# Performance work log

Measured on AMD Instinct MI355X. Metric: run time of the kernel, lower is better.

Reference implementation:

```python
import jax, jax.numpy as jnp
import numpy as np

EPS = 1e-8  # torch.nn.CosineSimilarity default eps


def setup_inputs() -> dict:
    key = jax.random.key(0)
    ks = jax.random.split(key, 6)
    B, N, SD, HD, AD = 512, 256, 1024, 512, 256
    return {
        "state_emb": jax.random.normal(ks[0], (B, SD), dtype=jnp.float32),
        "hints_emb": jax.random.normal(ks[1], (B, N, HD), dtype=jnp.float32),
        "Ws": jax.random.normal(ks[2], (AD, SD), dtype=jnp.float32) * 0.02,
        "bs": jax.random.normal(ks[3], (AD,), dtype=jnp.float32) * 0.02,
        "Wh": jax.random.normal(ks[4], (AD, HD), dtype=jnp.float32) * 0.02,
        "bh": jax.random.normal(ks[5], (AD,), dtype=jnp.float32) * 0.02,
    }


def reference(state_emb, hints_emb, Ws, bs, Wh, bh):
    # Projections
    sp = state_emb @ Ws.T + bs                       # (B, A)
    hp = jnp.einsum("bnh,ah->bna", hints_emb, Wh) + bh  # (B, N, A)
    # Cosine similarity along feature dim (torch CosineSimilarity semantics)
    sn = jnp.maximum(jnp.linalg.norm(sp, axis=-1, keepdims=True), EPS)    # (B,1)
    hn = jnp.maximum(jnp.linalg.norm(hp, axis=-1), EPS)                   # (B,N)
    scores = jnp.einsum("ba,bna->bn", sp, hp) / (sn * hn)                 # (B,N)
    attn_weights = jax.nn.softmax(scores, axis=1)                         # (B,N)
    # Weighted sum over hints (original, unprojected embeddings)
    output = jnp.einsum("bn,bnh->bh", attn_weights, hints_emb)            # (B,HD)
    return output
```

## Files before the change

### kernel.cpp

```cpp
#include <hip/hip_runtime.h>
#include <hip/hip_bf16.h>

typedef __attribute__((ext_vector_type(8))) short bf16x8;
typedef __attribute__((ext_vector_type(4))) float f32x4;

#define B_  512
#define N_  256
#define SD_ 1024
#define HD_ 512
#define AD_ 256

__device__ __forceinline__ unsigned short f2bf(float f) {
    unsigned int u = __float_as_uint(f);
    unsigned int r = (u + 0x7FFFu + ((u >> 16) & 1u)) >> 16;
    return (unsigned short)r;
}

__global__ void k0_pack(const float* __restrict__ Wh, unsigned short* __restrict__ whp) {
    int g = blockIdx.x * 256 + threadIdx.x;
    int ct  = g >> 10;
    int rem = g & 1023;
    int ks  = rem >> 6;
    int l   = rem & 63;
    int a   = ct * 16 + (l & 15);
    int kb  = ks * 32 + (l >> 4) * 8;
    const float* src = Wh + (size_t)a * HD_ + kb;
    float4 v0 = *(const float4*)(src);
    float4 v1 = *(const float4*)(src + 4);
    bf16x8 o;
    o[0] = (short)f2bf(v0.x); o[1] = (short)f2bf(v0.y);
    o[2] = (short)f2bf(v0.z); o[3] = (short)f2bf(v0.w);
    o[4] = (short)f2bf(v1.x); o[5] = (short)f2bf(v1.y);
    o[6] = (short)f2bf(v1.z); o[7] = (short)f2bf(v1.w);
    ((bf16x8*)whp)[g] = o;
}

__global__ __launch_bounds__(512) void k1_proj(
    const float* __restrict__ state, const float* __restrict__ Ws,
    const float* __restrict__ bs,
    float* __restrict__ sn, float* __restrict__ spv)
{
    __shared__ float st[2][SD_];
    __shared__ float spl[2][AD_];
    __shared__ float red[2][AD_];
    int tid = threadIdx.x, lane = tid & 63, w = tid >> 6;
    int b0 = blockIdx.x * 2;
    ((float4*)st)[tid] = ((const float4*)(state + (size_t)b0 * SD_))[tid];
    __syncthreads();
    float4 s0[4], s1[4];
    #pragma unroll
    for (int seg = 0; seg < 4; ++seg) {
        s0[seg] = *(const float4*)&st[0][seg * 256 + lane * 4];
        s1[seg] = *(const float4*)&st[1][seg * 256 + lane * 4];
    }
    #pragma unroll 2
    for (int i = 0; i < 32; ++i) {
        int a = w * 32 + i;
        const float4* wr = (const float4*)(Ws + (size_t)a * SD_);
        float p0 = 0.f, p1 = 0.f;
        #pragma unroll
        for (int seg = 0; seg < 4; ++seg) {
            float4 wv = wr[seg * 64 + lane];
            p0 += wv.x * s0[seg].x + wv.y * s0[seg].y + wv.z * s0[seg].z + wv.w * s0[seg].w;
            p1 += wv.x * s1[seg].x + wv.y * s1[seg].y + wv.z * s1[seg].z + wv.w * s1[seg].w;
        }
        #pragma unroll
        for (int d = 1; d < 64; d <<= 1) { p0 += __shfl_xor(p0, d); p1 += __shfl_xor(p1, d); }
        if (lane == 0) {
            float bsa = bs[a];
            spl[0][a] = p0 + bsa;
            spl[1][a] = p1 + bsa;
        }
    }
    __syncthreads();
    int tb = tid >> 8, t = tid & 255;
    float sv = spl[tb][t];
    spv[(size_t)(b0 + tb) * AD_ + t] = sv;
    red[tb][t] = sv * sv;
    __syncthreads();
    for (int s = 128; s > 0; s >>= 1) { if (t < s) red[tb][t] += red[tb][t + s]; __syncthreads(); }
    if (t == 0) sn[b0 + tb] = fmaxf(sqrtf(red[tb][0]), 1e-8f);
}

__global__ __launch_bounds__(512, 2) void k2_fused(
    const float* __restrict__ hints, const unsigned short* __restrict__ whp,
    const float* __restrict__ spv, const float* __restrict__ sn,
    const float* __restrict__ bh, float* __restrict__ out)
{
    __shared__ __align__(16) char smem[74752];
    unsigned short* tile = (unsigned short*)smem;
    float* sp_lds  = (float*)(smem + 65536);
    float* bh_lds  = (float*)(smem + 66560);
    float* norm2p  = (float*)(smem + 67584);
    float* nump    = (float*)(smem + 69632);
    float* sc      = (float*)(smem + 71680);
    float* red     = (float*)(smem + 72704);
    float* wsm     = (float*)(smem + 73728);
    float* scratch = (float*)smem;

    int tid = threadIdx.x, lane = tid & 63, w = tid >> 6;
    int b = blockIdx.x;
    const float* hb = hints + (size_t)b * N_ * HD_;
    if (tid < 64) ((float4*)sp_lds)[tid] = ((const float4*)(spv + (size_t)b * AD_))[tid];
    else if (tid < 128) ((float4*)bh_lds)[tid - 64] = ((const float4*)bh)[tid - 64];
    float snb = sn[b];
    int cl = lane & 15;
    int srow = tid >> 3;
    int sseg = tid & 7;
    const float* srcrow = hb + (size_t)srow * HD_ + sseg * 64;
    __syncthreads();
    float bh0 = bh_lds[(2 * w + 0) * 16 + cl];
    float bh1 = bh_lds[(2 * w + 1) * 16 + cl];
    float sp0 = sp_lds[(2 * w + 0) * 16 + cl];
    float sp1 = sp_lds[(2 * w + 1) * 16 + cl];

    #pragma unroll 1
    for (int mc = 0; mc < 4; ++mc) {
        const float* src = srcrow + (size_t)(mc * 64) * HD_;
        #pragma unroll
        for (int h = 0; h < 2; ++h) {
            float4 v[8];
            #pragma unroll
            for (int j = 0; j < 8; ++j)
                v[j] = *(const float4*)(src + h * 32 + j * 4);
            #pragma unroll
            for (int j2 = 0; j2 < 4; ++j2) {
                int s = sseg * 8 + h * 4 + j2;
                int sw = s ^ (srow & 15);
                float4 a = v[2 * j2], c = v[2 * j2 + 1];
                bf16x8 pk;
                pk[0] = (short)f2bf(a.x); pk[1] = (short)f2bf(a.y);
                pk[2] = (short)f2bf(a.z); pk[3] = (short)f2bf(a.w);
                pk[4] = (short)f2bf(c.x); pk[5] = (short)f2bf(c.y);
                pk[6] = (short)f2bf(c.z); pk[7] = (short)f2bf(c.w);
                *(bf16x8*)((char*)tile + srow * 1024 + sw * 16) = pk;
            }
        }
        __syncthreads();

        f32x4 acc[4][2];
        #pragma unroll
        for (int mf = 0; mf < 4; ++mf) {
            acc[mf][0] = (f32x4){0.f, 0.f, 0.f, 0.f};
            acc[mf][1] = (f32x4){0.f, 0.f, 0.f, 0.f};
        }
        #pragma unroll
        for (int kidx = 0; kidx < 16; ++kidx) {
            bf16x8 bfr0 = ((const bf16x8*)whp)[((2 * w + 0) * 16 + kidx) * 64 + lane];
            bf16x8 bfr1 = ((const bf16x8*)whp)[((2 * w + 1) * 16 + kidx) * 64 + lane];
            #pragma unroll
            for (int mf = 0; mf < 4; ++mf) {
                int r = mf * 16 + cl;
                int s = kidx * 4 + (lane >> 4);
                bf16x8 afr = *(const bf16x8*)((const char*)tile + r * 1024 +
                                              ((s ^ (r & 15)) << 4));
                acc[mf][0] = __builtin_amdgcn_mfma_f32_16x16x32_bf16(afr, bfr0, acc[mf][0], 0, 0, 0);
                acc[mf][1] = __builtin_amdgcn_mfma_f32_16x16x32_bf16(afr, bfr1, acc[mf][1], 0, 0, 0);
            }
        }

        #pragma unroll
        for (int mf = 0; mf < 4; ++mf) {
            #pragma unroll
            for (int r = 0; r < 4; ++r) {
                float h0 = acc[mf][0][r] + bh0;
                float h1 = acc[mf][1][r] + bh1;
                float vv = h0 * h0 + h1 * h1;
                float uu = sp0 * h0 + sp1 * h1;
                vv += __shfl_xor(vv, 1); uu += __shfl_xor(uu, 1);
                vv += __shfl_xor(vv, 2); uu += __shfl_xor(uu, 2);
                vv += __shfl_xor(vv, 4); uu += __shfl_xor(uu, 4);
                vv += __shfl_xor(vv, 8); uu += __shfl_xor(uu, 8);
                if (cl == 0) {
                    int idx = w * 64 + mf * 16 + (lane >> 4) * 4 + r;
                    norm2p[idx] = vv;
                    nump[idx]   = uu;
                }
            }
        }
        __syncthreads();
        if (tid < 64) {
            float n2 = 0.f, nm = 0.f;
            #pragma unroll
            for (int ww = 0; ww < 8; ++ww) {
                n2 += norm2p[ww * 64 + tid];
                nm += nump[ww * 64 + tid];
            }
            float hn = fmaxf(sqrtf(n2), 1e-8f);
            sc[mc * 64 + tid] = nm / (snb * hn);
        }
    }
    __syncthreads();

    if (tid < 256) red[tid] = sc[tid];
    __syncthreads();
    for (int s = 128; s > 0; s >>= 1) { if (tid < s) red[tid] = fmaxf(red[tid], red[tid + s]); __syncthreads(); }
    float mx = red[0];
    __syncthreads();
    if (tid < 256) { float e = __expf(sc[tid] - mx); sc[tid] = e; red[tid] = e; }
    __syncthreads();
    for (int s = 128; s > 0; s >>= 1) { if (tid < s) red[tid] += red[tid + s]; __syncthreads(); }
    float inv = 1.f / red[0];
    __syncthreads();
    if (tid < 256) wsm[tid] = sc[tid] * inv;
    __syncthreads();

    int hg = tid & 127, ng = tid >> 7;
    const float* hbe = hb + (size_t)(ng * 64) * HD_ + hg * 4;
    float ax = 0.f, ay = 0.f, az = 0.f, aw = 0.f;
    #pragma unroll 8
    for (int n = 0; n < 64; ++n) {
        float4 hv = *(const float4*)(hbe + (size_t)n * HD_);
        float wn = wsm[ng * 64 + n];
        ax += wn * hv.x; ay += wn * hv.y; az += wn * hv.z; aw += wn * hv.w;
    }
    *(float4*)(scratch + ng * 512 + hg * 4) = (float4){ax, ay, az, aw};
    __syncthreads();
    out[(size_t)b * HD_ + tid] =
        scratch[tid] + scratch[512 + tid] + scratch[1024 + tid] + scratch[1536 + tid];
}

extern "C" void kernel_launch(void* const* d_in, const int* in_sizes, int n_in,
                              void* d_out, int out_size, void* d_ws, size_t ws_size,
                              hipStream_t stream) {
    const float* state = (const float*)d_in[0];
    const float* hints = (const float*)d_in[1];
    const float* Ws    = (const float*)d_in[2];
    const float* bs    = (const float*)d_in[3];
    const float* Wh    = (const float*)d_in[4];
    const float* bh    = (const float*)d_in[5];
    float* out = (float*)d_out;

    float* sn = (float*)d_ws;
    float* spv = sn + B_;
    unsigned short* whp = (unsigned short*)(spv + (size_t)B_ * AD_);

    k0_pack<<<64, 256, 0, stream>>>(Wh, whp);
    k1_proj<<<B_ / 2, 512, 0, stream>>>(state, Ws, bs, sn, spv);
    k2_fused<<<B_, 512, 0, stream>>>(hints, whp, spv, sn, bh, out);
}
```

Baseline: 165.6 us.

## Split fused kernel into score and weighted-sum kernels with direct-register A loads

Replaces the single per-batch fused kernel with two kernels. The first runs four blocks per batch, each loading 64 hint rows straight from global memory into MFMA A fragments, converting them with the packed bf16 instruction instead of staging through LDS. The second does the softmax and weighted sum per batch. This adds parallelism and removes the LDS tile and its barriers. In exchange the hints tensor is read twice from HBM in separate launches, and the scores take an extra round trip through the workspace.

```diff
diff --git a/kernel.cpp b/kernel.cpp
--- a/kernel.cpp
+++ b/kernel.cpp
@@ -3,6 +3,7 @@
 
 typedef __attribute__((ext_vector_type(8))) short bf16x8;
 typedef __attribute__((ext_vector_type(4))) float f32x4;
+typedef __attribute__((ext_vector_type(4))) unsigned int u32x4;
 
 #define B_  512
 #define N_  256
@@ -14,6 +15,12 @@
     unsigned int u = __float_as_uint(f);
     unsigned int r = (u + 0x7FFFu + ((u >> 16) & 1u)) >> 16;
     return (unsigned short)r;
+}
+
+__device__ __forceinline__ unsigned int cvtpk(float lo, float hi) {
+    unsigned int r;
+    asm("v_cvt_pk_bf16_f32 %0, %1, %2" : "=v"(r) : "v"(lo), "v"(hi));
+    return r;
 }
 
 __global__ void k0_pack(const float* __restrict__ Wh, unsigned short* __restrict__ whp) {
@@ -82,116 +89,104 @@
     if (t == 0) sn[b0 + tb] = fmaxf(sqrtf(red[tb][0]), 1e-8f);
 }
 
-__global__ __launch_bounds__(512, 2) void k2_fused(
+__global__ __launch_bounds__(256, 3) void k2_scores(
     const float* __restrict__ hints, const unsigned short* __restrict__ whp,
     const float* __restrict__ spv, const float* __restrict__ sn,
-    const float* __restrict__ bh, float* __restrict__ out)
+    const float* __restrict__ bh, float* __restrict__ scores)
 {
-    __shared__ __align__(16) char smem[74752];
-    unsigned short* tile = (unsigned short*)smem;
-    float* sp_lds  = (float*)(smem + 65536);
-    float* bh_lds  = (float*)(smem + 66560);
-    float* norm2p  = (float*)(smem + 67584);
-    float* nump    = (float*)(smem + 69632);
-    float* sc      = (float*)(smem + 71680);
-    float* red     = (float*)(smem + 72704);
-    float* wsm     = (float*)(smem + 73728);
-    float* scratch = (float*)smem;
-
+    __shared__ float norm2p[4][64];
+    __shared__ float nump[4][64];
     int tid = threadIdx.x, lane = tid & 63, w = tid >> 6;
+    int blk = blockIdx.x;
+    int b = blk >> 2, m0 = (blk & 3) * 64;
+    const float* hb = hints + ((size_t)b * N_ + m0) * HD_;
+    int cl = lane & 15, q = lane >> 4;
+
+    float bhv[4], spc[4];
+    #pragma unroll
+    for (int ctl = 0; ctl < 4; ++ctl) {
+        int col = w * 64 + ctl * 16 + cl;
+        bhv[ctl] = bh[col];
+        spc[ctl] = spv[(size_t)b * AD_ + col];
+    }
+    float snb = sn[b];
+
+    f32x4 acc[4][4];
+    #pragma unroll
+    for (int mf = 0; mf < 4; ++mf)
+        #pragma unroll
+        for (int ctl = 0; ctl < 4; ++ctl) acc[mf][ctl] = (f32x4){0.f, 0.f, 0.f, 0.f};
+
+    const float* abase = hb + (size_t)cl * HD_ + q * 8;
+    const bf16x8* wp = (const bf16x8*)whp + (size_t)(w * 4) * 16 * 64 + lane;
+
+    #pragma unroll
+    for (int kidx = 0; kidx < 16; ++kidx) {
+        bf16x8 bfr[4];
+        #pragma unroll
+        for (int ctl = 0; ctl < 4; ++ctl)
+            bfr[ctl] = wp[(ctl * 16 + kidx) * 64];
+        #pragma unroll
+        for (int mf = 0; mf < 4; ++mf) {
+            const float* ap = abase + (size_t)(mf * 16) * HD_ + kidx * 32;
+            float4 a0 = *(const float4*)ap;
+            float4 a1 = *(const float4*)(ap + 4);
+            u32x4 t;
+            t[0] = cvtpk(a0.x, a0.y);
+            t[1] = cvtpk(a0.z, a0.w);
+            t[2] = cvtpk(a1.x, a1.y);
+            t[3] = cvtpk(a1.z, a1.w);
+            bf16x8 afr = __builtin_bit_cast(bf16x8, t);
+            #pragma unroll
+            for (int ctl = 0; ctl < 4; ++ctl)
+                acc[mf][ctl] = __builtin_amdgcn_mfma_f32_16x16x32_bf16(afr, bfr[ctl], acc[mf][ctl], 0, 0, 0);
+        }
+    }
+
+    #pragma unroll
+    for (int mf = 0; mf < 4; ++mf) {
+        #pragma unroll
+        for (int r = 0; r < 4; ++r) {
+            float vv = 0.f, uu = 0.f;
+            #pragma unroll
+            for (int ctl = 0; ctl < 4; ++ctl) {
+                float h = acc[mf][ctl][r] + bhv[ctl];
+                vv += h * h;
+                uu += spc[ctl] * h;
+            }
+            vv += __shfl_xor(vv, 1); uu += __shfl_xor(uu, 1);
+            vv += __shfl_xor(vv, 2); uu += __shfl_xor(uu, 2);
+            vv += __shfl_xor(vv, 4); uu += __shfl_xor(uu, 4);
+            vv += __shfl_xor(vv, 8); uu += __shfl_xor(uu, 8);
+            if (cl == 0) {
+                int row = mf * 16 + q * 4 + r;
+                norm2p[w][row] = vv;
+                nump[w][row]   = uu;
+            }
+        }
+    }
+    __syncthreads();
+    if (tid < 64) {
+        float n2 = norm2p[0][tid] + norm2p[1][tid] + norm2p[2][tid] + norm2p[3][tid];
+        float nm = nump[0][tid] + nump[1][tid] + nump[2][tid] + nump[3][tid];
+        float hn = fmaxf(sqrtf(n2), 1e-8f);
+        scores[(size_t)b * N_ + m0 + tid] = nm / (snb * hn);
+    }
+}
+
+__global__ __launch_bounds__(512) void k2b_out(
+    const float* __restrict__ hints, const float* __restrict__ scores,
+    float* __restrict__ out)
+{
+    __shared__ float sc[N_];
+    __shared__ float red[N_];
+    __shared__ float wsm[N_];
+    __shared__ float scratch[2048];
+    int tid = threadIdx.x;
     int b = blockIdx.x;
     const float* hb = hints + (size_t)b * N_ * HD_;
-    if (tid < 64) ((float4*)sp_lds)[tid] = ((const float4*)(spv + (size_t)b * AD_))[tid];
-    else if (tid < 128) ((float4*)bh_lds)[tid - 64] = ((const float4*)bh)[tid - 64];
-    float snb = sn[b];
-    int cl = lane & 15;
-    int srow = tid >> 3;
-    int sseg = tid & 7;
-    const float* srcrow = hb + (size_t)srow * HD_ + sseg * 64;
-    __syncthreads();
-    float bh0 = bh_lds[(2 * w + 0) * 16 + cl];
-    float bh1 = bh_lds[(2 * w + 1) * 16 + cl];
-    float sp0 = sp_lds[(2 * w + 0) * 16 + cl];
-    float sp1 = sp_lds[(2 * w + 1) * 16 + cl];
-
-    #pragma unroll 1
-    for (int mc = 0; mc < 4; ++mc) {
-        const float* src = srcrow + (size_t)(mc * 64) * HD_;
-        #pragma unroll
-        for (int h = 0; h < 2; ++h) {
-            float4 v[8];
-            #pragma unroll
-            for (int j = 0; j < 8; ++j)
-                v[j] = *(const float4*)(src + h * 32 + j * 4);
-            #pragma unroll
-            for (int j2 = 0; j2 < 4; ++j2) {
-                int s = sseg * 8 + h * 4 + j2;
-                int sw = s ^ (srow & 15);
-                float4 a = v[2 * j2], c = v[2 * j2 + 1];
-                bf16x8 pk;
-                pk[0] = (short)f2bf(a.x); pk[1] = (short)f2bf(a.y);
-                pk[2] = (short)f2bf(a.z); pk[3] = (short)f2bf(a.w);
-                pk[4] = (short)f2bf(c.x); pk[5] = (short)f2bf(c.y);
-                pk[6] = (short)f2bf(c.z); pk[7] = (short)f2bf(c.w);
-                *(bf16x8*)((char*)tile + srow * 1024 + sw * 16) = pk;
-            }
-        }
-        __syncthreads();
-
-        f32x4 acc[4][2];
-        #pragma unroll
-        for (int mf = 0; mf < 4; ++mf) {
-            acc[mf][0] = (f32x4){0.f, 0.f, 0.f, 0.f};
-            acc[mf][1] = (f32x4){0.f, 0.f, 0.f, 0.f};
-        }
-        #pragma unroll
-        for (int kidx = 0; kidx < 16; ++kidx) {
-            bf16x8 bfr0 = ((const bf16x8*)whp)[((2 * w + 0) * 16 + kidx) * 64 + lane];
-            bf16x8 bfr1 = ((const bf16x8*)whp)[((2 * w + 1) * 16 + kidx) * 64 + lane];
-            #pragma unroll
-            for (int mf = 0; mf < 4; ++mf) {
-                int r = mf * 16 + cl;
-                int s = kidx * 4 + (lane >> 4);
-                bf16x8 afr = *(const bf16x8*)((const char*)tile + r * 1024 +
-                                              ((s ^ (r & 15)) << 4));
-                acc[mf][0] = __builtin_amdgcn_mfma_f32_16x16x32_bf16(afr, bfr0, acc[mf][0], 0, 0, 0);
-                acc[mf][1] = __builtin_amdgcn_mfma_f32_16x16x32_bf16(afr, bfr1, acc[mf][1], 0, 0, 0);
-            }
-        }
-
-        #pragma unroll
-        for (int mf = 0; mf < 4; ++mf) {
-            #pragma unroll
-            for (int r = 0; r < 4; ++r) {
-                float h0 = acc[mf][0][r] + bh0;
-                float h1 = acc[mf][1][r] + bh1;
-                float vv = h0 * h0 + h1 * h1;
-                float uu = sp0 * h0 + sp1 * h1;
-                vv += __shfl_xor(vv, 1); uu += __shfl_xor(uu, 1);
-                vv += __shfl_xor(vv, 2); uu += __shfl_xor(uu, 2);
-                vv += __shfl_xor(vv, 4); uu += __shfl_xor(uu, 4);
-                vv += __shfl_xor(vv, 8); uu += __shfl_xor(uu, 8);
-                if (cl == 0) {
-                    int idx = w * 64 + mf * 16 + (lane >> 4) * 4 + r;
-                    norm2p[idx] = vv;
-                    nump[idx]   = uu;
-                }
-            }
-        }
-        __syncthreads();
-        if (tid < 64) {
-            float n2 = 0.f, nm = 0.f;
-            #pragma unroll
-            for (int ww = 0; ww < 8; ++ww) {
-                n2 += norm2p[ww * 64 + tid];
-                nm += nump[ww * 64 + tid];
-            }
-            float hn = fmaxf(sqrtf(n2), 1e-8f);
-            sc[mc * 64 + tid] = nm / (snb * hn);
-        }
-    }
-    __syncthreads();
-
+    if (tid < 256) sc[tid] = scores[(size_t)b * N_ + tid];
+    __syncthreads();
     if (tid < 256) red[tid] = sc[tid];
     __syncthreads();
     for (int s = 128; s > 0; s >>= 1) { if (tid < s) red[tid] = fmaxf(red[tid], red[tid + s]); __syncthreads(); }
@@ -234,8 +229,10 @@
     float* sn = (float*)d_ws;
     float* spv = sn + B_;
     unsigned short* whp = (unsigned short*)(spv + (size_t)B_ * AD_);
+    float* scores = (float*)(whp + (size_t)AD_ * HD_);
 
     k0_pack<<<64, 256, 0, stream>>>(Wh, whp);
     k1_proj<<<B_ / 2, 512, 0, stream>>>(state, Ws, bs, sn, spv);
-    k2_fused<<<B_, 512, 0, stream>>>(hints, whp, spv, sn, bh, out);
-}
+    k2_scores<<<B_ * 4, 256, 0, stream>>>(hints, whp, spv, sn, bh, scores);
+    k2b_out<<<B_, 512, 0, stream>>>(hints, scores, out);
+}
```

Measured after the change: 223.4 us. +34.9%, slower.
